# Optimization experiments

Hardware: AMD Instinct MI355X
Metric: run time of the kernel (lower is better)

## Reference

```python
import jax, jax.numpy as jnp
import numpy as np

N = 100000      # nodes
E = 1600000     # edges (before self loops)
G = 64          # graphs (drones)
H = 4           # heads
C = 64          # hidden_channels (per-head dim, concat=False)
NODE_F = 32
DRONE_F = 16
OUT = 32
L = 2           # num_layers
LN_EPS = 1e-5
NEG_SLOPE = 0.2


def setup_inputs() -> dict:
    key = jax.random.key(0)
    ks = jax.random.split(key, 20)
    gn = lambda k, shape, s=0.1: jax.random.normal(k, shape, jnp.float32) * s
    inp = {}
    inp["x"] = jax.random.normal(ks[0], (N, NODE_F), jnp.float32)
    inp["drone_feat"] = jax.random.normal(ks[1], (G, DRONE_F), jnp.float32)
    inp["edge_index"] = jax.random.randint(ks[2], (2, E), 0, N, jnp.int32)
    inp["batch"] = jnp.sort(jax.random.randint(ks[3], (N,), 0, G, jnp.int32))
    inp["node_W"] = gn(ks[4], (C, NODE_F)); inp["node_b"] = jnp.zeros((C,), jnp.float32)
    inp["drone_W"] = gn(ks[5], (C, DRONE_F)); inp["drone_b"] = jnp.zeros((C,), jnp.float32)
    for l in range(L):
        kk = jax.random.split(ks[6 + l], 3)
        inp[f"convW{l}"] = gn(kk[0], (H * C, C))
        inp[f"att_src{l}"] = gn(kk[1], (H, C))
        inp[f"att_dst{l}"] = gn(kk[2], (H, C))
        inp[f"convb{l}"] = jnp.zeros((C,), jnp.float32)
        inp[f"ln_g{l}"] = jnp.ones((C,), jnp.float32)
        inp[f"ln_b{l}"] = jnp.zeros((C,), jnp.float32)
    inp["out_W"] = gn(ks[10], (OUT, C)); inp["out_b"] = jnp.zeros((OUT,), jnp.float32)
    return inp


def _layer_norm(x, g, b):
    mu = jnp.mean(x, axis=-1, keepdims=True)
    var = jnp.mean((x - mu) ** 2, axis=-1, keepdims=True)
    return (x - mu) * jax.lax.rsqrt(var + LN_EPS) * g + b


def _gat_conv(h, src, dst, W, a_src, a_dst, b):
    # h: [N, C] -> per-head transform [N, H, C]
    xh = (h @ W.T).reshape(N, H, C)
    alpha_s = jnp.sum(xh * a_src[None], axis=-1)  # [N, H]
    alpha_d = jnp.sum(xh * a_dst[None], axis=-1)  # [N, H]
    e = jax.nn.leaky_relu(alpha_s[src] + alpha_d[dst], NEG_SLOPE)  # [E', H]
    m = jax.ops.segment_max(e, dst, num_segments=N)  # segment softmax over dst
    ex = jnp.exp(e - m[dst])
    s = jax.ops.segment_sum(ex, dst, num_segments=N)
    alpha = ex / (s[dst] + 1e-16)                   # [E', H]
    out = jax.ops.segment_sum(xh[src] * alpha[:, :, None], dst, num_segments=N)
    return jnp.mean(out, axis=1) + b                # concat=False -> head mean


def reference(x, edge_index, drone_feat, batch, node_W, node_b, drone_W, drone_b,
              convW0, att_src0, att_dst0, convb0, ln_g0, ln_b0,
              convW1, att_src1, att_dst1, convb1, ln_g1, ln_b1,
              out_W, out_b):
    # add self loops (PyG GATConv default add_self_loops=True)
    loop = jnp.arange(N, dtype=edge_index.dtype)
    src = jnp.concatenate([edge_index[0], loop])
    dst = jnp.concatenate([edge_index[1], loop])
    h = x @ node_W.T + node_b + (drone_feat @ drone_W.T + drone_b)[batch]
    layers = [(convW0, att_src0, att_dst0, convb0, ln_g0, ln_b0),
              (convW1, att_src1, att_dst1, convb1, ln_g1, ln_b1)]
    for (W, a_s, a_d, cb, g, lb) in layers:
        h = h + jax.nn.relu(_layer_norm(_gat_conv(h, src, dst, W, a_s, a_d, cb), g, lb))
    return h @ out_W.T + out_b
```

## Files before the change

kernel.cpp:

```cpp
#include <hip/hip_runtime.h>
#include <hip/hip_fp16.h>
#include <math.h>


#define NEG_SLOPE 0.2f
#define LN_EPS 1e-5f

struct __align__(8) h16x4 { __half x, y, z, w; };

__global__ __launch_bounds__(256) void k_h0(
        const float* __restrict__ x, const int* __restrict__ batch,
        const float* __restrict__ node_W, const float* __restrict__ drone_W,
        const float* __restrict__ node_b, const float* __restrict__ drone_b,
        const float* __restrict__ drone_feat,
        float* __restrict__ h, int* __restrict__ cnt, int N) {
    __shared__ float xs[16][33];
    __shared__ float ds[16][17];
    __shared__ float wn[32][65];
    __shared__ float wd[16][65];
    __shared__ float bs[64];
    int t = threadIdx.x;
    int n0 = blockIdx.x * 16;
    for (int i = t; i < 2048; i += 256) { int co = i >> 5, k = i & 31; wn[k][co] = node_W[i]; }
    for (int i = t; i < 1024; i += 256) { int co = i >> 4, k = i & 15; wd[k][co] = drone_W[i]; }
    if (t < 64) bs[t] = node_b[t] + drone_b[t];
    for (int i = t; i < 512; i += 256) {
        int r = i >> 5, c = i & 31;
        int n = n0 + r;
        xs[r][c] = (n < N) ? x[(size_t)n * 32 + c] : 0.f;
    }
    {
        int r = t >> 4, c = t & 15;
        int n = n0 + r;
        int g = (n < N) ? batch[n] : 0;
        ds[r][c] = drone_feat[g * 16 + c];
    }
    {
        int gt = blockIdx.x * 256 + t;
        if (gt < N) cnt[gt] = 0;
    }
    __syncthreads();
    int co = t & 63;
    int nsub = t >> 6;
    float b = bs[co];
    float a0 = b, a1 = b, a2 = b, a3 = b;
#pragma unroll
    for (int k = 0; k < 32; ++k) {
        float w = wn[k][co];
        a0 = fmaf(xs[nsub * 4 + 0][k], w, a0);
        a1 = fmaf(xs[nsub * 4 + 1][k], w, a1);
        a2 = fmaf(xs[nsub * 4 + 2][k], w, a2);
        a3 = fmaf(xs[nsub * 4 + 3][k], w, a3);
    }
#pragma unroll
    for (int k = 0; k < 16; ++k) {
        float w = wd[k][co];
        a0 = fmaf(ds[nsub * 4 + 0][k], w, a0);
        a1 = fmaf(ds[nsub * 4 + 1][k], w, a1);
        a2 = fmaf(ds[nsub * 4 + 2][k], w, a2);
        a3 = fmaf(ds[nsub * 4 + 3][k], w, a3);
    }
    float av[4] = {a0, a1, a2, a3};
#pragma unroll
    for (int j = 0; j < 4; ++j) {
        int n = n0 + nsub * 4 + j;
        if (n < N) h[(size_t)n * 64 + co] = av[j];
    }
}

__global__ void k_scatter(const int* __restrict__ edge_index, int* __restrict__ cnt,
                          int* __restrict__ csrB,
                          const float* __restrict__ cW0, const float* __restrict__ cW1,
                          const float* __restrict__ s0, const float* __restrict__ d0,
                          const float* __restrict__ s1, const float* __restrict__ d1,
                          const float* __restrict__ out_W,
                          float* __restrict__ wt0, float* __restrict__ wt1,
                          float* __restrict__ uv, float* __restrict__ owT,
                          int E) {
    if (blockIdx.x < 128) {
        int i = blockIdx.x * 256 + threadIdx.x;
        {
            int j = i & 16383;
            int co = j >> 6, k = j & 63;
            if (i < 16384) wt0[k * 256 + co] = cW0[j];
            else           wt1[k * 256 + co] = cW1[j];
        }
        if (i < 2048) {
            int k = i >> 5, o = i & 31;
            owT[i] = out_W[o * 64 + k];
        }
        if (i < 1024) {
            int l = i >> 9, sd = (i >> 8) & 1, head = (i >> 6) & 3, kk = i & 63;
            const float* W   = l ? cW1 : cW0;
            const float* att = l ? (sd ? d1 : s1) : (sd ? d0 : s0);
            float acc = 0.f;
            for (int c = 0; c < 64; ++c)
                acc += W[(head * 64 + c) * 64 + kk] * att[head * 64 + c];
            uv[i] = acc;
        }
    }
    int i = (blockIdx.x * blockDim.x + threadIdx.x) * 4;
    if (i + 3 < E) {
        int4 sv = *(const int4*)(edge_index + i);
        int4 dv = *(const int4*)(edge_index + E + i);
        int sl;
        sl = atomicAdd(cnt + dv.x, 1); if (sl < 63) csrB[((size_t)dv.x << 6) + 1 + sl] = sv.x;
        sl = atomicAdd(cnt + dv.y, 1); if (sl < 63) csrB[((size_t)dv.y << 6) + 1 + sl] = sv.y;
        sl = atomicAdd(cnt + dv.z, 1); if (sl < 63) csrB[((size_t)dv.z << 6) + 1 + sl] = sv.z;
        sl = atomicAdd(cnt + dv.w, 1); if (sl < 63) csrB[((size_t)dv.w << 6) + 1 + sl] = sv.w;
    } else {
        for (int k = i; k < E; ++k) {
            int d = edge_index[E + k];
            int sl = atomicAdd(cnt + d, 1);
            if (sl < 63) csrB[((size_t)d << 6) + 1 + sl] = edge_index[k];
        }
    }
}

#define XPAD 68
__global__ __launch_bounds__(256) void k_xh(
        const float* __restrict__ h, const float* __restrict__ wt,
        const float* __restrict__ uv_l, __half* __restrict__ xh,
        float* __restrict__ as_, float* __restrict__ ad_, int N) {
    __shared__ float hs[32][XPAD];
    int t = threadIdx.x;
    int n0 = blockIdx.x * 32;
    for (int i = t; i < 32 * 64; i += 256) {
        int r = i >> 6, c = i & 63;
        int n = n0 + r;
        hs[r][c] = (n < N) ? h[(size_t)n * 64 + c] : 0.f;
    }
    __syncthreads();
    int co4 = (t & 63) * 4;
    int nsub = t >> 6;
    float4 acc[8];
#pragma unroll
    for (int j = 0; j < 8; ++j) acc[j] = make_float4(0.f, 0.f, 0.f, 0.f);
    const float* wp = wt + co4;
#pragma unroll 2
    for (int k4 = 0; k4 < 16; ++k4) {
        float4 w0 = *(const float4*)(wp + (k4 * 4 + 0) * 256);
        float4 w1 = *(const float4*)(wp + (k4 * 4 + 1) * 256);
        float4 w2 = *(const float4*)(wp + (k4 * 4 + 2) * 256);
        float4 w3 = *(const float4*)(wp + (k4 * 4 + 3) * 256);
#pragma unroll
        for (int j = 0; j < 8; ++j) {
            float4 hv = *(const float4*)&hs[nsub * 8 + j][k4 * 4];
            float4 a = acc[j];
            a.x = fmaf(hv.x, w0.x, fmaf(hv.y, w1.x, fmaf(hv.z, w2.x, fmaf(hv.w, w3.x, a.x))));
            a.y = fmaf(hv.x, w0.y, fmaf(hv.y, w1.y, fmaf(hv.z, w2.y, fmaf(hv.w, w3.y, a.y))));
            a.z = fmaf(hv.x, w0.z, fmaf(hv.y, w1.z, fmaf(hv.z, w2.z, fmaf(hv.w, w3.z, a.z))));
            a.w = fmaf(hv.x, w0.w, fmaf(hv.y, w1.w, fmaf(hv.z, w2.w, fmaf(hv.w, w3.w, a.w))));
            acc[j] = a;
        }
    }
#pragma unroll
    for (int j = 0; j < 8; ++j) {
        int n = n0 + nsub * 8 + j;
        if (n < N) {
            h16x4 o;
            o.x = __float2half(acc[j].x);
            o.y = __float2half(acc[j].y);
            o.z = __float2half(acc[j].z);
            o.w = __float2half(acc[j].w);
            *(h16x4*)(xh + (size_t)n * 256 + co4) = o;
        }
    }
    {
        int row  = t >> 3;
        int head = (t >> 1) & 3;
        int sd   = t & 1;
        int n = n0 + row;
        if (n < N) {
            const float* u = uv_l + sd * 256 + head * 64;
            float a = 0.f;
#pragma unroll
            for (int k4 = 0; k4 < 16; ++k4) {
                float4 hv = *(const float4*)&hs[row][k4 * 4];
                float4 uu = *(const float4*)(u + k4 * 4);
                a += hv.x * uu.x + hv.y * uu.y + hv.z * uu.z + hv.w * uu.w;
            }
            (sd ? ad_ : as_)[n * 4 + head] = a;
        }
    }
}

__device__ __forceinline__ __half2 shxor_h2(__half2 a, int m) {
    int u = __shfl_xor(*(int*)&a, m, 64);
    return *(__half2*)&u;
}

template <bool LAST>
__global__ __launch_bounds__(256) void k_gat(
        const __half* __restrict__ xh, const float* __restrict__ as_,
        const float* __restrict__ ad_, const int* __restrict__ cnt,
        const int* __restrict__ csrB, const float* __restrict__ convb,
        const float* __restrict__ ln_g, const float* __restrict__ ln_b,
        float* __restrict__ h, const float* __restrict__ owT,
        const float* __restrict__ out_b, float* __restrict__ out, int N) {
    __shared__ float owT_lds[2048];
    __shared__ float hout_lds4[4][64];
    int t = threadIdx.x;
    int wid = t >> 6, lane = t & 63;
    if (LAST) {
        for (int i = t; i < 2048; i += 256) owT_lds[i] = owT[i];
        __syncthreads();
    }
    int n = blockIdx.x * 4 + wid;
    if (n >= N) return;
    float* hout_lds = hout_lds4[wid];
    int g    = lane >> 4;
    int l16  = lane & 15;
    int head = l16 >> 2;
    int r0 = n << 6;
    int r1 = r0 + 1 + min(cnt[n], 63);
    float adv = ad_[(size_t)n * 4 + head];
    const char* xbb = (const char*)xh + (l16 << 5);
    const char* asb = (const char*)as_ + (head << 2);
    const char* cbb = (const char*)csrB;

    float s = 0.f;
    __half2 acc[8];
#pragma unroll
    for (int j = 0; j < 8; ++j) acc[j] = __float2half2_rn(0.f);

    uint4 zero4 = make_uint4(0u, 0u, 0u, 0u);
    int idx;
    idx = r0 + g;      bool vA = idx < r1; int sA = n; if (g != 0 && vA) sA = *(const int*)(cbb + ((unsigned)idx << 2));
    idx = r0 + 4 + g;  bool vB = idx < r1; int sB = 0; if (vB) sB = *(const int*)(cbb + ((unsigned)idx << 2));
    idx = r0 + 8 + g;  bool vC = idx < r1; int sC = 0; if (vC) sC = *(const int*)(cbb + ((unsigned)idx << 2));
    idx = r0 + 12 + g; bool vD = idx < r1; int sD = 0; if (vD) sD = *(const int*)(cbb + ((unsigned)idx << 2));
    float asA = 0.f, asB = 0.f;
    uint4 qA0 = zero4, qA1 = zero4, qB0 = zero4, qB1 = zero4;
    if (vA) {
        asA = *(const float*)(asb + ((unsigned)sA << 4));
        const uint4* bp = (const uint4*)(xbb + ((unsigned)sA << 9));
        qA0 = bp[0]; qA1 = bp[1];
    }
    if (vB) {
        asB = *(const float*)(asb + ((unsigned)sB << 4));
        const uint4* bp = (const uint4*)(xbb + ((unsigned)sB << 9));
        qB0 = bp[0]; qB1 = bp[1];
    }

    auto COMPUTE = [&](bool vc, float asc, const uint4& q0, const uint4& q1) {
        float e = asc + adv;
        e = e > 0.f ? e : NEG_SLOPE * e;
        float w = __expf(e);
        w = vc ? w : 0.f;
        s += w;
        __half2 w2 = __float2half2_rn(w);
        const __half2* ha = (const __half2*)&q0;
        const __half2* hb = (const __half2*)&q1;
        acc[0] = __hfma2(w2, ha[0], acc[0]);
        acc[1] = __hfma2(w2, ha[1], acc[1]);
        acc[2] = __hfma2(w2, ha[2], acc[2]);
        acc[3] = __hfma2(w2, ha[3], acc[3]);
        acc[4] = __hfma2(w2, hb[0], acc[4]);
        acc[5] = __hfma2(w2, hb[1], acc[5]);
        acc[6] = __hfma2(w2, hb[2], acc[6]);
        acc[7] = __hfma2(w2, hb[3], acc[7]);
    };

    for (int i = r0; i < r1; i += 8) {
        COMPUTE(vA, asA, qA0, qA1);
        int idxE = i + 16 + g; bool vE = idxE < r1; int sE = 0;
        if (vE) sE = *(const int*)(cbb + ((unsigned)idxE << 2));
        vA = vC;
        if (vC) {
            asA = *(const float*)(asb + ((unsigned)sC << 4));
            const uint4* bp = (const uint4*)(xbb + ((unsigned)sC << 9));
            qA0 = bp[0]; qA1 = bp[1];
        }
        COMPUTE(vB, asB, qB0, qB1);
        int idxF = i + 20 + g; bool vF = idxF < r1; int sF = 0;
        if (vF) sF = *(const int*)(cbb + ((unsigned)idxF << 2));
        vB = vD;
        if (vD) {
            asB = *(const float*)(asb + ((unsigned)sD << 4));
            const uint4* bp = (const uint4*)(xbb + ((unsigned)sD << 9));
            qB0 = bp[0]; qB1 = bp[1];
        }
        vC = vE; sC = sE;
        vD = vF; sD = sF;
    }

    s += __shfl_xor(s, 16, 64);
    s += __shfl_xor(s, 32, 64);
#pragma unroll
    for (int j = 0; j < 8; ++j) {
        acc[j] = __hadd2(acc[j], shxor_h2(acc[j], 16));
        acc[j] = __hadd2(acc[j], shxor_h2(acc[j], 32));
    }
    float inv = 1.f / (s + 1e-16f);
    __half2 ih = __float2half2_rn(inv);
#pragma unroll
    for (int j = 0; j < 8; ++j) {
        acc[j] = __hmul2(acc[j], ih);
        acc[j] = __hadd2(acc[j], shxor_h2(acc[j], 4));
        acc[j] = __hadd2(acc[j], shxor_h2(acc[j], 8));
    }
    float f[16];
#pragma unroll
    for (int j = 0; j < 8; ++j) {
        float2 tv = __half22float2(acc[j]);
        f[2 * j]     = tv.x;
        f[2 * j + 1] = tv.y;
    }
    int cblk = lane & 3;
    int cb16 = cblk * 16;
    float o[16];
    float part = 0.f;
#pragma unroll
    for (int q = 0; q < 4; ++q) {
        float4 cb = *(const float4*)(convb + cb16 + q * 4);
        o[q * 4 + 0] = 0.25f * f[q * 4 + 0] + cb.x;
        o[q * 4 + 1] = 0.25f * f[q * 4 + 1] + cb.y;
        o[q * 4 + 2] = 0.25f * f[q * 4 + 2] + cb.z;
        o[q * 4 + 3] = 0.25f * f[q * 4 + 3] + cb.w;
        part += o[q * 4 + 0] + o[q * 4 + 1] + o[q * 4 + 2] + o[q * 4 + 3];
    }
    part += __shfl_xor(part, 1, 64);
    part += __shfl_xor(part, 2, 64);
    float mu = part * (1.f / 64.f);
    float vs = 0.f;
#pragma unroll
    for (int j = 0; j < 16; ++j) { o[j] -= mu; vs += o[j] * o[j]; }
    vs += __shfl_xor(vs, 1, 64);
    vs += __shfl_xor(vs, 2, 64);
    float rstd = rsqrtf(vs * (1.f / 64.f) + LN_EPS);

    if (!LAST) {
        if (lane < 4) {
            float4* hp = (float4*)(h + (size_t)n * 64 + cb16);
#pragma unroll
            for (int q = 0; q < 4; ++q) {
                float4 hv = hp[q];
                float4 gv = *(const float4*)(ln_g + cb16 + q * 4);
                float4 bv = *(const float4*)(ln_b + cb16 + q * 4);
                hv.x += fmaxf(o[q * 4 + 0] * rstd * gv.x + bv.x, 0.f);
                hv.y += fmaxf(o[q * 4 + 1] * rstd * gv.y + bv.y, 0.f);
                hv.z += fmaxf(o[q * 4 + 2] * rstd * gv.z + bv.z, 0.f);
                hv.w += fmaxf(o[q * 4 + 3] * rstd * gv.w + bv.w, 0.f);
                hp[q] = hv;
            }
        }
    } else {
        if (lane < 4) {
            const float4* hp = (const float4*)(h + (size_t)n * 64 + cb16);
#pragma unroll
            for (int q = 0; q < 4; ++q) {
                float4 hv = hp[q];
                float4 gv = *(const float4*)(ln_g + cb16 + q * 4);
                float4 bv = *(const float4*)(ln_b + cb16 + q * 4);
                hout_lds[cb16 + q * 4 + 0] = hv.x + fmaxf(o[q * 4 + 0] * rstd * gv.x + bv.x, 0.f);
                hout_lds[cb16 + q * 4 + 1] = hv.y + fmaxf(o[q * 4 + 1] * rstd * gv.y + bv.y, 0.f);
                hout_lds[cb16 + q * 4 + 2] = hv.z + fmaxf(o[q * 4 + 2] * rstd * gv.z + bv.z, 0.f);
                hout_lds[cb16 + q * 4 + 3] = hv.w + fmaxf(o[q * 4 + 3] * rstd * gv.w + bv.w, 0.f);
            }
        }
        asm volatile("s_waitcnt lgkmcnt(0)" ::: "memory");
        if (lane < 32) {
            float acc2 = out_b[lane];
#pragma unroll 8
            for (int k = 0; k < 64; ++k)
                acc2 = fmaf(hout_lds[k], owT_lds[k * 32 + lane], acc2);
            out[(size_t)n * 32 + lane] = acc2;
        }
    }
}

static inline unsigned cdiv(long long a, long long b) { return (unsigned)((a + b - 1) / b); }

extern "C" void kernel_launch(void* const* d_in, const int* in_sizes, int n_in,
                              void* d_out, int out_size, void* d_ws, size_t ws_size,
                              hipStream_t stream) {
    const float* x          = (const float*)d_in[0];
    const float* drone_feat = (const float*)d_in[1];
    const int*   edge_index = (const int*)d_in[2];
    const int*   batch      = (const int*)d_in[3];
    const float* node_W     = (const float*)d_in[4];
    const float* node_b     = (const float*)d_in[5];
    const float* drone_W    = (const float*)d_in[6];
    const float* drone_b    = (const float*)d_in[7];
    const float* convW[2]   = {(const float*)d_in[8],  (const float*)d_in[14]};
    const float* att_src[2] = {(const float*)d_in[9],  (const float*)d_in[15]};
    const float* att_dst[2] = {(const float*)d_in[10], (const float*)d_in[16]};
    const float* convb[2]   = {(const float*)d_in[11], (const float*)d_in[17]};
    const float* ln_g[2]    = {(const float*)d_in[12], (const float*)d_in[18]};
    const float* ln_b[2]    = {(const float*)d_in[13], (const float*)d_in[19]};
    const float* out_W      = (const float*)d_in[20];
    const float* out_b      = (const float*)d_in[21];
    float* out = (float*)d_out;

    const int N = in_sizes[0] / 32;
    const int E = in_sizes[2] / 2;

    char* base = (char*)d_ws;
    size_t off = 0;
    auto alloc = [&](size_t bytes) {
        char* p = base + off;
        off = (off + bytes + 255) & ~(size_t)255;
        return p;
    };
    float*           h      = (float*)alloc((size_t)N * 64 * 4);
    __half*          xh     = (__half*)alloc((size_t)N * 256 * 2);
    float*           as_    = (float*)alloc((size_t)N * 4 * 4);
    float*           ad_    = (float*)alloc((size_t)N * 4 * 4);
    float*           wt0    = (float*)alloc((size_t)256 * 64 * 4);
    float*           wt1    = (float*)alloc((size_t)256 * 64 * 4);
    float*           uv     = (float*)alloc((size_t)1024 * 4);
    float*           owT    = (float*)alloc((size_t)2048 * 4);
    int*             cnt    = (int*)alloc((size_t)N * 4);
    int*             csrB   = (int*)alloc((size_t)N * 64 * 4);
    (void)ws_size;
    const float* wt[2] = {wt0, wt1};

    k_h0<<<cdiv(N, 16), 256, 0, stream>>>(x, batch, node_W, drone_W, node_b, drone_b,
                                          drone_feat, h, cnt, N);
    k_scatter<<<cdiv(cdiv(E, 4), 256), 256, 0, stream>>>(
        edge_index, cnt, csrB,
        convW[0], convW[1], att_src[0], att_dst[0],
        att_src[1], att_dst[1], out_W,
        wt0, wt1, uv, owT, E);
    k_xh<<<cdiv(N, 32), 256, 0, stream>>>(h, wt[0], uv + 0 * 512, xh, as_, ad_, N);
    k_gat<false><<<cdiv(N, 4), 256, 0, stream>>>(xh, as_, ad_, cnt, csrB, convb[0],
                                                 ln_g[0], ln_b[0], h, owT, out_b, out, N);
    k_xh<<<cdiv(N, 32), 256, 0, stream>>>(h, wt[1], uv + 1 * 512, xh, as_, ad_, N);
    k_gat<true><<<cdiv(N, 4), 256, 0, stream>>>(xh, as_, ad_, cnt, csrB, convb[1],
                                                ln_g[1], ln_b[1], h, owT, out_b, out, N);
}
```

Before: 727.2 us.

## Fuse input projection into first xh kernel and partition edge scatter by destination range

Removes the separate h0 kernel by computing the initial node embedding inside the first k_xh instance (template FIRST), writing h both to shared memory and global, and replaces the cnt zeroing with a memset. The edge scatter grid gains a second dimension of 8 destination partitions; each partition rereads all edges but only does atomics for its destination range, aiming to improve locality of the cnt atomics and csrB writes. The trade-off is eightfold edge_index reads and more launched blocks in exchange for cache-friendlier atomic traffic and one fewer kernel launch.

```diff
diff --git a/kernel.cpp b/kernel.cpp
--- a/kernel.cpp
+++ b/kernel.cpp
@@ -7,66 +7,6 @@
 #define LN_EPS 1e-5f
 
 struct __align__(8) h16x4 { __half x, y, z, w; };
-
-__global__ __launch_bounds__(256) void k_h0(
-        const float* __restrict__ x, const int* __restrict__ batch,
-        const float* __restrict__ node_W, const float* __restrict__ drone_W,
-        const float* __restrict__ node_b, const float* __restrict__ drone_b,
-        const float* __restrict__ drone_feat,
-        float* __restrict__ h, int* __restrict__ cnt, int N) {
-    __shared__ float xs[16][33];
-    __shared__ float ds[16][17];
-    __shared__ float wn[32][65];
-    __shared__ float wd[16][65];
-    __shared__ float bs[64];
-    int t = threadIdx.x;
-    int n0 = blockIdx.x * 16;
-    for (int i = t; i < 2048; i += 256) { int co = i >> 5, k = i & 31; wn[k][co] = node_W[i]; }
-    for (int i = t; i < 1024; i += 256) { int co = i >> 4, k = i & 15; wd[k][co] = drone_W[i]; }
-    if (t < 64) bs[t] = node_b[t] + drone_b[t];
-    for (int i = t; i < 512; i += 256) {
-        int r = i >> 5, c = i & 31;
-        int n = n0 + r;
-        xs[r][c] = (n < N) ? x[(size_t)n * 32 + c] : 0.f;
-    }
-    {
-        int r = t >> 4, c = t & 15;
-        int n = n0 + r;
-        int g = (n < N) ? batch[n] : 0;
-        ds[r][c] = drone_feat[g * 16 + c];
-    }
-    {
-        int gt = blockIdx.x * 256 + t;
-        if (gt < N) cnt[gt] = 0;
-    }
-    __syncthreads();
-    int co = t & 63;
-    int nsub = t >> 6;
-    float b = bs[co];
-    float a0 = b, a1 = b, a2 = b, a3 = b;
-#pragma unroll
-    for (int k = 0; k < 32; ++k) {
-        float w = wn[k][co];
-        a0 = fmaf(xs[nsub * 4 + 0][k], w, a0);
-        a1 = fmaf(xs[nsub * 4 + 1][k], w, a1);
-        a2 = fmaf(xs[nsub * 4 + 2][k], w, a2);
-        a3 = fmaf(xs[nsub * 4 + 3][k], w, a3);
-    }
-#pragma unroll
-    for (int k = 0; k < 16; ++k) {
-        float w = wd[k][co];
-        a0 = fmaf(ds[nsub * 4 + 0][k], w, a0);
-        a1 = fmaf(ds[nsub * 4 + 1][k], w, a1);
-        a2 = fmaf(ds[nsub * 4 + 2][k], w, a2);
-        a3 = fmaf(ds[nsub * 4 + 3][k], w, a3);
-    }
-    float av[4] = {a0, a1, a2, a3};
-#pragma unroll
-    for (int j = 0; j < 4; ++j) {
-        int n = n0 + nsub * 4 + j;
-        if (n < N) h[(size_t)n * 64 + co] = av[j];
-    }
-}
 
 __global__ void k_scatter(const int* __restrict__ edge_index, int* __restrict__ cnt,
                           int* __restrict__ csrB,
@@ -76,8 +16,8 @@
                           const float* __restrict__ out_W,
                           float* __restrict__ wt0, float* __restrict__ wt1,
                           float* __restrict__ uv, float* __restrict__ owT,
-                          int E) {
-    if (blockIdx.x < 128) {
+                          int E, int S) {
+    if (blockIdx.y == 0 && blockIdx.x < 128) {
         int i = blockIdx.x * 256 + threadIdx.x;
         {
             int j = i & 16383;
@@ -99,38 +39,84 @@
             uv[i] = acc;
         }
     }
+    int lo = blockIdx.y * S, hi = lo + S;
     int i = (blockIdx.x * blockDim.x + threadIdx.x) * 4;
     if (i + 3 < E) {
         int4 sv = *(const int4*)(edge_index + i);
         int4 dv = *(const int4*)(edge_index + E + i);
         int sl;
-        sl = atomicAdd(cnt + dv.x, 1); if (sl < 63) csrB[((size_t)dv.x << 6) + 1 + sl] = sv.x;
-        sl = atomicAdd(cnt + dv.y, 1); if (sl < 63) csrB[((size_t)dv.y << 6) + 1 + sl] = sv.y;
-        sl = atomicAdd(cnt + dv.z, 1); if (sl < 63) csrB[((size_t)dv.z << 6) + 1 + sl] = sv.z;
-        sl = atomicAdd(cnt + dv.w, 1); if (sl < 63) csrB[((size_t)dv.w << 6) + 1 + sl] = sv.w;
+        if (dv.x >= lo && dv.x < hi) { sl = atomicAdd(cnt + dv.x, 1); if (sl < 63) csrB[((size_t)dv.x << 6) + 1 + sl] = sv.x; }
+        if (dv.y >= lo && dv.y < hi) { sl = atomicAdd(cnt + dv.y, 1); if (sl < 63) csrB[((size_t)dv.y << 6) + 1 + sl] = sv.y; }
+        if (dv.z >= lo && dv.z < hi) { sl = atomicAdd(cnt + dv.z, 1); if (sl < 63) csrB[((size_t)dv.z << 6) + 1 + sl] = sv.z; }
+        if (dv.w >= lo && dv.w < hi) { sl = atomicAdd(cnt + dv.w, 1); if (sl < 63) csrB[((size_t)dv.w << 6) + 1 + sl] = sv.w; }
     } else {
         for (int k = i; k < E; ++k) {
             int d = edge_index[E + k];
-            int sl = atomicAdd(cnt + d, 1);
-            if (sl < 63) csrB[((size_t)d << 6) + 1 + sl] = edge_index[k];
+            if (d >= lo && d < hi) {
+                int sl = atomicAdd(cnt + d, 1);
+                if (sl < 63) csrB[((size_t)d << 6) + 1 + sl] = edge_index[k];
+            }
         }
     }
 }
 
 #define XPAD 68
+template <bool FIRST>
 __global__ __launch_bounds__(256) void k_xh(
         const float* __restrict__ h, const float* __restrict__ wt,
         const float* __restrict__ uv_l, __half* __restrict__ xh,
-        float* __restrict__ as_, float* __restrict__ ad_, int N) {
+        float* __restrict__ as_, float* __restrict__ ad_,
+        const float* __restrict__ x, const int* __restrict__ batch,
+        const float* __restrict__ node_W, const float* __restrict__ drone_W,
+        const float* __restrict__ node_b, const float* __restrict__ drone_b,
+        const float* __restrict__ drone_feat, float* __restrict__ h_out, int N) {
     __shared__ float hs[32][XPAD];
+    __shared__ float wn[FIRST ? 32 : 1][FIRST ? 65 : 1];
+    __shared__ float wd[FIRST ? 16 : 1][FIRST ? 65 : 1];
+    __shared__ float bs[FIRST ? 64 : 1];
+    __shared__ float xs[FIRST ? 32 : 1][FIRST ? 33 : 1];
+    __shared__ float ds[FIRST ? 32 : 1][FIRST ? 17 : 1];
     int t = threadIdx.x;
     int n0 = blockIdx.x * 32;
-    for (int i = t; i < 32 * 64; i += 256) {
-        int r = i >> 6, c = i & 63;
-        int n = n0 + r;
-        hs[r][c] = (n < N) ? h[(size_t)n * 64 + c] : 0.f;
-    }
-    __syncthreads();
+    if constexpr (FIRST) {
+        for (int i = t; i < 2048; i += 256) { int co = i >> 5, k = i & 31; wn[k][co] = node_W[i]; }
+        for (int i = t; i < 1024; i += 256) { int co = i >> 4, k = i & 15; wd[k][co] = drone_W[i]; }
+        if (t < 64) bs[t] = node_b[t] + drone_b[t];
+        for (int i = t; i < 1024; i += 256) {
+            int r = i >> 5, c = i & 31;
+            int n = n0 + r;
+            xs[r][c] = (n < N) ? x[(size_t)n * 32 + c] : 0.f;
+        }
+        for (int i = t; i < 512; i += 256) {
+            int r = i >> 4, c = i & 15;
+            int n = n0 + r;
+            int g = (n < N) ? batch[n] : 0;
+            ds[r][c] = drone_feat[g * 16 + c];
+        }
+        __syncthreads();
+        int co = t & 63, nsub = t >> 6;
+        float b = bs[co];
+#pragma unroll
+        for (int j = 0; j < 8; ++j) {
+            int r = nsub * 8 + j;
+            float a = b;
+#pragma unroll
+            for (int k = 0; k < 32; ++k) a = fmaf(xs[r][k], wn[k][co], a);
+#pragma unroll
+            for (int k = 0; k < 16; ++k) a = fmaf(ds[r][k], wd[k][co], a);
+            hs[r][co] = a;
+            int n = n0 + r;
+            if (n < N) h_out[(size_t)n * 64 + co] = a;
+        }
+        __syncthreads();
+    } else {
+        for (int i = t; i < 32 * 64; i += 256) {
+            int r = i >> 6, c = i & 63;
+            int n = n0 + r;
+            hs[r][c] = (n < N) ? h[(size_t)n * 64 + c] : 0.f;
+        }
+        __syncthreads();
+    }
     int co4 = (t & 63) * 4;
     int nsub = t >> 6;
     float4 acc[8];
@@ -395,6 +381,8 @@
 
     const int N = in_sizes[0] / 32;
     const int E = in_sizes[2] / 2;
+    const int P = 8;
+    const int S = cdiv(N, P);
 
     char* base = (char*)d_ws;
     size_t off = 0;
@@ -416,17 +404,22 @@
     (void)ws_size;
     const float* wt[2] = {wt0, wt1};
 
-    k_h0<<<cdiv(N, 16), 256, 0, stream>>>(x, batch, node_W, drone_W, node_b, drone_b,
-                                          drone_feat, h, cnt, N);
-    k_scatter<<<cdiv(cdiv(E, 4), 256), 256, 0, stream>>>(
-        edge_index, cnt, csrB,
-        convW[0], convW[1], att_src[0], att_dst[0],
-        att_src[1], att_dst[1], out_W,
-        wt0, wt1, uv, owT, E);
-    k_xh<<<cdiv(N, 32), 256, 0, stream>>>(h, wt[0], uv + 0 * 512, xh, as_, ad_, N);
+    (void)hipMemsetAsync(cnt, 0, (size_t)N * 4, stream);
+    {
+        dim3 g(cdiv(cdiv(E, 4), 256), P);
+        k_scatter<<<g, 256, 0, stream>>>(edge_index, cnt, csrB,
+                                         convW[0], convW[1], att_src[0], att_dst[0],
+                                         att_src[1], att_dst[1], out_W,
+                                         wt0, wt1, uv, owT, E, S);
+    }
+    k_xh<true><<<cdiv(N, 32), 256, 0, stream>>>(h, wt[0], uv + 0 * 512, xh, as_, ad_,
+                                                x, batch, node_W, drone_W, node_b,
+                                                drone_b, drone_feat, h, N);
     k_gat<false><<<cdiv(N, 4), 256, 0, stream>>>(xh, as_, ad_, cnt, csrB, convb[0],
                                                  ln_g[0], ln_b[0], h, owT, out_b, out, N);
-    k_xh<<<cdiv(N, 32), 256, 0, stream>>>(h, wt[1], uv + 1 * 512, xh, as_, ad_, N);
+    k_xh<false><<<cdiv(N, 32), 256, 0, stream>>>(h, wt[1], uv + 1 * 512, xh, as_, ad_,
+                                                 x, batch, node_W, drone_W, node_b,
+                                                 drone_b, drone_feat, h, N);
     k_gat<true><<<cdiv(N, 4), 256, 0, stream>>>(xh, as_, ad_, cnt, csrB, convb[1],
                                                 ln_g[1], ln_b[1], h, owT, out_b, out, N);
 }
```

After: 632.2 us. -13.1%, faster.
